# Kernel optimization log

Measured on AMD Instinct MI355X. Metric: run time of the kernel, lower is better.

The kernel has to match this reference:

```python
import jax, jax.numpy as jnp
import numpy as np

# pywt Wavelet('db4') decomposition filters (8 taps)
DEC_LO = jnp.array([-0.010597401784997278, 0.032883011666982945, 0.030841381835986965,
                    -0.18703481171888114, -0.02798376941698385, 0.6308807679295904,
                    0.7148465705525415, 0.23037781330885523], dtype=jnp.float32)
DEC_HI = jnp.array([-0.23037781330885523, 0.7148465705525415, -0.6308807679295904,
                    -0.02798376941698385, 0.18703481171888114, 0.030841381835986965,
                    -0.032883011666982945, -0.010597401784997278], dtype=jnp.float32)
FLEN = 8
LEVEL = 3


def _dwt_last(x, f):
    """Single-level DWT along last axis, pywt 'symmetric' mode.
    out[i] = sum_k f[k] * ext[2i+1-k] (true convolution, downsample by 2)."""
    p = FLEN - 1
    pad = [(0, 0)] * (x.ndim - 1) + [(p, p)]
    xp = jnp.pad(x, pad, mode='symmetric')[..., 1:]
    n = x.shape[-1]
    out_len = (n + FLEN - 1) // 2
    f_rev = f[::-1]
    y = f_rev[0] * xp[..., 0:2 * out_len:2]
    for j in range(1, FLEN):  # fixed 8-tap loop
        y = y + f_rev[j] * xp[..., j:j + 2 * out_len:2]
    return y


def _dwt_h(x, f):
    # DWT along axis -2 (rows/H)
    return jnp.swapaxes(_dwt_last(jnp.swapaxes(x, -1, -2), f), -1, -2)


def _dwt2(x):
    # x: [B, H, W] -> (cA, cH, cV, cD), matching pywt dwt2 ('aa','da','ad','dd')
    lo_w = _dwt_last(x, DEC_LO)
    hi_w = _dwt_last(x, DEC_HI)
    cA = _dwt_h(lo_w, DEC_LO)  # low H,  low W
    cH = _dwt_h(lo_w, DEC_HI)  # high H, low W  (horizontal detail)
    cV = _dwt_h(hi_w, DEC_LO)  # low H,  high W (vertical detail)
    cD = _dwt_h(hi_w, DEC_HI)  # high H, high W (diagonal detail)
    return cA, cH, cV, cD


def setup_inputs() -> dict:
    key = jax.random.key(0)
    x = jax.random.normal(key, (16, 1, 1024, 1024), dtype=jnp.float32)
    return {"x": x}


def reference(x):
    # wavedec2 ordering: (cA_L, (cH_L, cV_L, cD_L), ..., (cH_1, cV_1, cD_1))
    a = x[:, 0]  # [B, H, W]
    details = []
    for _ in range(LEVEL):
        a, lh, hl, hh = _dwt2(a)
        details.insert(0, (lh, hl, hh))  # coarsest first, as pywt returns
    outs = [a[:, None]]  # [B,1,h,w]
    for lh, hl, hh in details:
        outs += [lh[:, None], hl[:, None], hh[:, None]]
    return tuple(outs)
```

## Files before the change

kernel.cpp:

```cpp
#include <hip/hip_runtime.h>

typedef float f4 __attribute__((ext_vector_type(4)));
typedef f4 f4u __attribute__((aligned(4)));

__device__ __forceinline__ int refl(int i, int n) {
    i = (i < 0) ? (-i - 1) : i;
    i = (i >= n) ? (2 * n - 1 - i) : i;
    return i;
}

__device__ __forceinline__ unsigned bpack(float lo, float hi) {
    union { float f; unsigned u; } a, b;
    a.f = lo; b.f = hi;
    const unsigned ua = (a.u + 0x7FFFu + ((a.u >> 16) & 1u)) >> 16;
    const unsigned ub = (b.u + 0x7FFFu + ((b.u >> 16) & 1u)) & 0xFFFF0000u;
    return ua | ub;
}
__device__ __forceinline__ float b_lo(unsigned u) {
    union { unsigned u; float f; } x; x.u = u << 16; return x.f;
}
__device__ __forceinline__ float b_hi(unsigned u) {
    union { unsigned u; float f; } x; x.u = u & 0xFFFF0000u; return x.f;
}

__device__ __constant__ const float LOF[8] = {
    -0.010597401784997278f,  0.032883011666982945f,
     0.030841381835986965f, -0.18703481171888114f,
    -0.02798376941698385f,   0.6308807679295904f,
     0.7148465705525415f,    0.23037781330885523f };
__device__ __constant__ const float HIF[8] = {
    -0.23037781330885523f,   0.7148465705525415f,
    -0.6308807679295904f,   -0.02798376941698385f,
     0.18703481171888114f,   0.030841381835986965f,
    -0.032883011666982945f, -0.010597401784997278f };

template<int N, int LDIN, int M>
__global__ __launch_bounds__(256, 3)
void dwt_stripe(const float* __restrict__ in, int inb,
                float* __restrict__ oA, int ldA, int Ab,
                float* __restrict__ oH, float* __restrict__ oV,
                float* __restrict__ oD)
{
    constexpr int NG  = (M + 7) / 8;
    constexpr int LDP = 8 * NG;
    constexpr int S   = (M + 3) / 4;
    constexpr int NA  = 14 * NG;
    constexpr int NQF = M / 4;
    constexpr int TC  = M - 4 * NQF;
    constexpr int NB  = 2 * NQF + 2 * TC;

    __shared__ unsigned s[14 * LDP];

    const int G = gridDim.x;
    const int q = G >> 3, rm = G & 7;
    const int xcd = blockIdx.x & 7, pos = blockIdx.x >> 3;
    const int sid = xcd * q + (xcd < rm ? xcd : rm) + pos;
    const int sy = sid % S, b = sid / S;

    const int tid = threadIdx.x;
    const int gr0 = 4 * sy;
    const int rb  = 2 * gr0 - 6;
    const float* Ain = in + b * inb;

    #pragma unroll
    for (int k = 0; k < (NA + 255) / 256; ++k) {
        const int item = k * 256 + tid;
        if (item < NA) {
            const int trow = item / NG, g = item - trow * NG;
            const int ri = rb + trow;
            const int cb = 16 * g - 8;
            float v[24];
            if (ri >= 0 && ri < N && g >= 1 && 16 * g + 15 < N) {
                const float* p = Ain + ri * LDIN + cb;
                #pragma unroll
                for (int j = 0; j < 6; ++j) {
                    const float4 t4 = *(const float4*)(p + 4 * j);
                    v[4*j] = t4.x; v[4*j+1] = t4.y; v[4*j+2] = t4.z; v[4*j+3] = t4.w;
                }
            } else {
                const float* row = Ain + refl(ri, N) * LDIN;
                #pragma unroll
                for (int u = 0; u < 24; ++u) v[u] = row[refl(cb + u, N)];
            }
            unsigned w[8];
            #pragma unroll
            for (int d = 0; d < 8; ++d) {
                float lo = 0.f, hi = 0.f;
                #pragma unroll
                for (int t = 0; t < 8; ++t) {
                    const float x = v[2 * d + 9 - t];
                    lo += LOF[t] * x;
                    hi += HIF[t] * x;
                }
                w[d] = bpack(lo, hi);
            }
            unsigned* dst = &s[trow * LDP + 8 * g];
            *(uint4*)(dst)     = make_uint4(w[0], w[1], w[2], w[3]);
            *(uint4*)(dst + 4) = make_uint4(w[4], w[5], w[6], w[7]);
        }
    }
    __syncthreads();

    #pragma unroll
    for (int k = 0; k < (NB + 255) / 256; ++k) {
        const int item = k * 256 + tid;
        if (item < 2 * NQF) {
            const int pr = item / NQF, qc = item - pr * NQF;
            uint4 qv[10];
            #pragma unroll
            for (int j = 0; j < 10; ++j)
                qv[j] = *(const uint4*)&s[(4 * pr + j) * LDP + 4 * qc];

            #pragma unroll
            for (int d = 0; d < 2; ++d) {
                const int gr = gr0 + 2 * pr + d;
                if (gr >= M) continue;
                f4 vA = 0.f, vH = 0.f, vV = 0.f, vD = 0.f;
                #pragma unroll
                for (int t = 0; t < 8; ++t) {
                    const uint4 qq = qv[2 * d + 7 - t];
                    f4 lo, hi;
                    lo.x = b_lo(qq.x); lo.y = b_lo(qq.y); lo.z = b_lo(qq.z); lo.w = b_lo(qq.w);
                    hi.x = b_hi(qq.x); hi.y = b_hi(qq.y); hi.z = b_hi(qq.z); hi.w = b_hi(qq.w);
                    vA += LOF[t] * lo;  vH += HIF[t] * lo;
                    vV += LOF[t] * hi;  vD += HIF[t] * hi;
                }
                const int cq = 4 * qc;
                *(f4u*)&oA[b * Ab + gr * ldA + cq] = vA;
                const int od = b * (M * M) + gr * M + cq;
                *(f4u*)&oH[od] = vH;
                *(f4u*)&oV[od] = vV;
                *(f4u*)&oD[od] = vD;
            }
        } else if (item < NB) {
            const int e = item - 2 * NQF;
            const int pr = e & 1, c = 4 * NQF + (e >> 1);
            float lov[10], hiv[10];
            #pragma unroll
            for (int j = 0; j < 10; ++j) {
                const unsigned u = s[(4 * pr + j) * LDP + c];
                lov[j] = b_lo(u); hiv[j] = b_hi(u);
            }
            float A0=0.f,H0=0.f,V0=0.f,D0=0.f,A1=0.f,H1=0.f,V1=0.f,D1=0.f;
            #pragma unroll
            for (int t = 0; t < 8; ++t) {
                const float l0 = lov[7 - t], h0 = hiv[7 - t];
                const float l1 = lov[9 - t], h1 = hiv[9 - t];
                A0 += LOF[t] * l0;  H0 += HIF[t] * l0;
                V0 += LOF[t] * h0;  D0 += HIF[t] * h0;
                A1 += LOF[t] * l1;  H1 += HIF[t] * l1;
                V1 += LOF[t] * h1;  D1 += HIF[t] * h1;
            }
            const int gr = gr0 + 2 * pr;
            const int od = b * (M * M) + gr * M + c;
            if (gr < M) {
                oA[b * Ab + gr * ldA + c] = A0;
                oH[od] = H0; oV[od] = V0; oD[od] = D0;
            }
            if (gr + 1 < M) {
                oA[b * Ab + (gr + 1) * ldA + c] = A1;
                oH[od + M] = H1; oV[od + M] = V1; oD[od + M] = D1;
            }
        }
    }
}

#define NTF 512
__global__ __launch_bounds__(NTF, 8)
void dwt2_fused(const float* __restrict__ in, int n, int ldin, int inb,
                int m, int nty, int ntx,
                float* __restrict__ oA, int ldA, int Ab,
                float* __restrict__ oH, float* __restrict__ oV,
                float* __restrict__ oD)
{
    __shared__ unsigned s[70 * 36];

    const int G = gridDim.x;
    const int q = G >> 3, rm = G & 7;
    const int xcd = blockIdx.x & 7, pos = blockIdx.x >> 3;
    const int i = xcd * q + (xcd < rm ? xcd : rm) + pos;
    const int ty = i % nty;
    const int t2 = i / nty;
    const int tx = t2 % ntx;
    const int b  = t2 / ntx;

    const int tid = threadIdx.x;
    const int c0 = tx * 32, r0 = ty * 32;
    const float* Ain = in + b * inb;

    const int rb  = 2 * r0 - 6;
    const int cw0 = 2 * c0 - 8;
    const bool interior = (rb >= 0) && (rb + 69 < n) && (cw0 >= 0) && (cw0 + 71 < n);

    const int tr0 = tid >> 3, g0 = tid & 7;
    const bool has2 = (tid < 48);
    const int tr1 = 64 + (tid >> 3), g1 = tid & 7;

    float v0[16], v1[16];
    if (interior) {
        const float* p0 = Ain + (rb + tr0) * ldin + (cw0 + 8 * g0);
        const float4 a0 = ((const float4*)p0)[0];
        const float4 a1 = ((const float4*)p0)[1];
        const float4 a2 = ((const float4*)p0)[2];
        const float4 a3 = ((const float4*)p0)[3];
        v0[0]=a0.x; v0[1]=a0.y; v0[2]=a0.z; v0[3]=a0.w;
        v0[4]=a1.x; v0[5]=a1.y; v0[6]=a1.z; v0[7]=a1.w;
        v0[8]=a2.x; v0[9]=a2.y; v0[10]=a2.z; v0[11]=a2.w;
        v0[12]=a3.x; v0[13]=a3.y; v0[14]=a3.z; v0[15]=a3.w;
        if (has2) {
            const float* p1 = Ain + (rb + tr1) * ldin + (cw0 + 8 * g1);
            const float4 b0 = ((const float4*)p1)[0];
            const float4 b1 = ((const float4*)p1)[1];
            const float4 b2 = ((const float4*)p1)[2];
            const float4 b3 = ((const float4*)p1)[3];
            v1[0]=b0.x; v1[1]=b0.y; v1[2]=b0.z; v1[3]=b0.w;
            v1[4]=b1.x; v1[5]=b1.y; v1[6]=b1.z; v1[7]=b1.w;
            v1[8]=b2.x; v1[9]=b2.y; v1[10]=b2.z; v1[11]=b2.w;
            v1[12]=b3.x; v1[13]=b3.y; v1[14]=b3.z; v1[15]=b3.w;
        }
    } else {
        const float* row0 = Ain + refl(rb + tr0, n) * ldin;
        const int cb0 = cw0 + 8 * g0;
        #pragma unroll
        for (int u = 0; u < 16; ++u) v0[u] = row0[refl(cb0 + u, n)];
        if (has2) {
            const float* row1 = Ain + refl(rb + tr1, n) * ldin;
            const int cb1 = cw0 + 8 * g1;
            #pragma unroll
            for (int u = 0; u < 16; ++u) v1[u] = row1[refl(cb1 + u, n)];
        }
    }

    {
        unsigned w[4];
        #pragma unroll
        for (int d = 0; d < 4; ++d) {
            float lo = 0.f, hi = 0.f;
            #pragma unroll
            for (int t = 0; t < 8; ++t) {
                const float x = v0[2 * d + 9 - t];
                lo += LOF[t] * x;
                hi += HIF[t] * x;
            }
            w[d] = bpack(lo, hi);
        }
        *(uint4*)&s[tr0 * 36 + 4 * g0] = make_uint4(w[0], w[1], w[2], w[3]);
    }
    if (has2) {
        unsigned w[4];
        #pragma unroll
        for (int d = 0; d < 4; ++d) {
            float lo = 0.f, hi = 0.f;
            #pragma unroll
            for (int t = 0; t < 8; ++t) {
                const float x = v1[2 * d + 9 - t];
                lo += LOF[t] * x;
                hi += HIF[t] * x;
            }
            w[d] = bpack(lo, hi);
        }
        *(uint4*)&s[tr1 * 36 + 4 * g1] = make_uint4(w[0], w[1], w[2], w[3]);
    }
    __syncthreads();

    const int c = tid & 31, pr = tid >> 5;
    float lov[10], hiv[10];
    #pragma unroll
    for (int j = 0; j < 10; ++j) {
        const unsigned u = s[(4 * pr + j) * 36 + c];
        lov[j] = b_lo(u); hiv[j] = b_hi(u);
    }
    float A0=0.f,H0=0.f,V0=0.f,D0=0.f,A1=0.f,H1=0.f,V1=0.f,D1=0.f;
    #pragma unroll
    for (int t = 0; t < 8; ++t) {
        const float l0 = lov[7 - t], h0 = hiv[7 - t];
        const float l1 = lov[9 - t], h1 = hiv[9 - t];
        A0 += LOF[t] * l0;  H0 += HIF[t] * l0;
        V0 += LOF[t] * h0;  D0 += HIF[t] * h0;
        A1 += LOF[t] * l1;  H1 += HIF[t] * l1;
        V1 += LOF[t] * h1;  D1 += HIF[t] * h1;
    }
    const int gr = r0 + 2 * pr, gc = c0 + c;
    if (gc < m) {
        const int ob = b * (m * m);
        const int od = ob + gr * m + gc;
        if (gr < m) {
            oA[b * Ab + gr * ldA + gc] = A0;
            oH[od] = H0; oV[od] = V0; oD[od] = D0;
        }
        if (gr + 1 < m) {
            oA[b * Ab + (gr + 1) * ldA + gc] = A1;
            oH[od + m] = H1; oV[od + m] = V1; oD[od + m] = D1;
        }
    }
}

extern "C" void kernel_launch(void* const* d_in, const int* in_sizes, int n_in,
                              void* d_out, int out_size, void* d_ws, size_t ws_size,
                              hipStream_t stream) {
    const float* x = (const float*)d_in[0];
    float* out = (float*)d_out;
    float* ws  = (float*)d_ws;

    const int B = 16;
    const int m1 = 515, m2 = 261, m3 = 134;
    const int n2 = 515, n3 = 261;

    const int ld1 = 516, b1 = m1 * ld1;
    const int ld2 = 264, b2 = m2 * ld2;
    float* a1 = ws;
    float* a2 = ws + (size_t)b1 * B;

    const size_t sz1 = (size_t)B * m1 * m1;
    const size_t sz2 = (size_t)B * m2 * m2;
    const size_t sz3 = (size_t)B * m3 * m3;

    float* a3  = out;
    float* lh3 = a3  + sz3;
    float* hl3 = lh3 + sz3;
    float* hh3 = hl3 + sz3;
    float* lh2 = hh3 + sz3;
    float* hl2 = lh2 + sz2;
    float* hh2 = hl2 + sz2;
    float* lh1 = hh2 + sz2;
    float* hl1 = lh1 + sz1;
    float* hh1 = hl1 + sz1;

    const int S1 = (m1 + 3) / 4;
    const int t2_ = (m2 + 31) / 32;
    const int t3  = (m3 + 31) / 32;

    dim3 blk(256);
    dwt_stripe<1024, 1024, 515><<<dim3(S1 * B), blk, 0, stream>>>(
        x, 1024 * 1024, a1, ld1, b1, lh1, hl1, hh1);

    dwt2_fused<<<dim3(t2_ * t2_ * B), dim3(NTF), 0, stream>>>(
        a1, n2, ld1, b1, m2, t2_, t2_,
        a2, ld2, b2, lh2, hl2, hh2);

    dwt2_fused<<<dim3(t3 * t3 * B), dim3(NTF), 0, stream>>>(
        a2, n3, ld2, b2, m3, t3, t3,
        a3, m3, m3 * m3, lh3, hl3, hh3);
}
```

Baseline: 56.75 us.

## Process eight output rows per stripe block and split interior/edge loads

The first-level stripe kernel is parameterised by rows per block and now computes 8 output rows instead of 4. This cuts the redundant 6-row vertical halo recomputed by each block relative to useful rows. The horizontal pass is also split so interior column groups always take the vectorised float4 path with only row reflection, and the two edge groups use the scalar reflected path. The cost is more shared memory per block (22 rows) and half as many blocks, which may reduce occupancy or parallelism.

```diff
diff --git a/kernel.cpp b/kernel.cpp
--- a/kernel.cpp
+++ b/kernel.cpp
@@ -34,7 +34,7 @@
      0.18703481171888114f,   0.030841381835986965f,
     -0.032883011666982945f, -0.010597401784997278f };
 
-template<int N, int LDIN, int M>
+template<int N, int LDIN, int M, int RPB>
 __global__ __launch_bounds__(256, 3)
 void dwt_stripe(const float* __restrict__ in, int inb,
                 float* __restrict__ oA, int ldA, int Ab,
@@ -43,13 +43,20 @@
 {
     constexpr int NG  = (M + 7) / 8;
     constexpr int LDP = 8 * NG;
-    constexpr int S   = (M + 3) / 4;
-    constexpr int NA  = 14 * NG;
+    constexpr int S   = (M + RPB - 1) / RPB;
+    constexpr int HR  = 2 * RPB + 6;
+    constexpr int GHI = (N - 16) / 16;
+    constexpr int NGI = GHI;
+    static_assert(NG - 1 == GHI + 1, "expect exactly 2 edge groups");
+    constexpr int NAI = HR * NGI;
+    constexpr int NAT = NAI + HR * 2;
     constexpr int NQF = M / 4;
     constexpr int TC  = M - 4 * NQF;
-    constexpr int NB  = 2 * NQF + 2 * TC;
-
-    __shared__ unsigned s[14 * LDP];
+    constexpr int NBM = (RPB / 2) * NQF;
+    constexpr int NBT2 = (RPB / 2) * TC;
+    constexpr int NB  = NBM + NBT2;
+
+    __shared__ unsigned s[HR * LDP];
 
     const int G = gridDim.x;
     const int q = G >> 3, rm = G & 7;
@@ -58,29 +65,23 @@
     const int sy = sid % S, b = sid / S;
 
     const int tid = threadIdx.x;
-    const int gr0 = 4 * sy;
+    const int gr0 = RPB * sy;
     const int rb  = 2 * gr0 - 6;
     const float* Ain = in + b * inb;
 
     #pragma unroll
-    for (int k = 0; k < (NA + 255) / 256; ++k) {
+    for (int k = 0; k < (NAT + 255) / 256; ++k) {
         const int item = k * 256 + tid;
-        if (item < NA) {
-            const int trow = item / NG, g = item - trow * NG;
-            const int ri = rb + trow;
-            const int cb = 16 * g - 8;
+        if (item < NAI) {
+            const int tr = item / NGI;
+            const int g  = 1 + (item - tr * NGI);
+            const int rr = refl(rb + tr, N);
+            const float* p = Ain + rr * LDIN + (16 * g - 8);
             float v[24];
-            if (ri >= 0 && ri < N && g >= 1 && 16 * g + 15 < N) {
-                const float* p = Ain + ri * LDIN + cb;
-                #pragma unroll
-                for (int j = 0; j < 6; ++j) {
-                    const float4 t4 = *(const float4*)(p + 4 * j);
-                    v[4*j] = t4.x; v[4*j+1] = t4.y; v[4*j+2] = t4.z; v[4*j+3] = t4.w;
-                }
-            } else {
-                const float* row = Ain + refl(ri, N) * LDIN;
-                #pragma unroll
-                for (int u = 0; u < 24; ++u) v[u] = row[refl(cb + u, N)];
+            #pragma unroll
+            for (int j = 0; j < 6; ++j) {
+                const float4 t4 = *(const float4*)(p + 4 * j);
+                v[4*j] = t4.x; v[4*j+1] = t4.y; v[4*j+2] = t4.z; v[4*j+3] = t4.w;
             }
             unsigned w[8];
             #pragma unroll
@@ -94,7 +95,32 @@
                 }
                 w[d] = bpack(lo, hi);
             }
-            unsigned* dst = &s[trow * LDP + 8 * g];
+            unsigned* dst = &s[tr * LDP + 8 * g];
+            *(uint4*)(dst)     = make_uint4(w[0], w[1], w[2], w[3]);
+            *(uint4*)(dst + 4) = make_uint4(w[4], w[5], w[6], w[7]);
+        } else if (item < NAT) {
+            const int e  = item - NAI;
+            const int tr = e >> 1;
+            const int g  = (e & 1) ? (GHI + 1) : 0;
+            const int rr = refl(rb + tr, N);
+            const float* row = Ain + rr * LDIN;
+            const int cb = 16 * g - 8;
+            float v[24];
+            #pragma unroll
+            for (int u = 0; u < 24; ++u) v[u] = row[refl(cb + u, N)];
+            unsigned w[8];
+            #pragma unroll
+            for (int d = 0; d < 8; ++d) {
+                float lo = 0.f, hi = 0.f;
+                #pragma unroll
+                for (int t = 0; t < 8; ++t) {
+                    const float x = v[2 * d + 9 - t];
+                    lo += LOF[t] * x;
+                    hi += HIF[t] * x;
+                }
+                w[d] = bpack(lo, hi);
+            }
+            unsigned* dst = &s[tr * LDP + 8 * g];
             *(uint4*)(dst)     = make_uint4(w[0], w[1], w[2], w[3]);
             *(uint4*)(dst + 4) = make_uint4(w[4], w[5], w[6], w[7]);
         }
@@ -104,7 +130,7 @@
     #pragma unroll
     for (int k = 0; k < (NB + 255) / 256; ++k) {
         const int item = k * 256 + tid;
-        if (item < 2 * NQF) {
+        if (item < NBM) {
             const int pr = item / NQF, qc = item - pr * NQF;
             uint4 qv[10];
             #pragma unroll
@@ -133,8 +159,8 @@
                 *(f4u*)&oD[od] = vD;
             }
         } else if (item < NB) {
-            const int e = item - 2 * NQF;
-            const int pr = e & 1, c = 4 * NQF + (e >> 1);
+            const int e = item - NBM;
+            const int pr = e % (RPB / 2), c = 4 * NQF + e / (RPB / 2);
             float lov[10], hiv[10];
             #pragma unroll
             for (int j = 0; j < 10; ++j) {
@@ -326,12 +352,12 @@
     float* hl1 = lh1 + sz1;
     float* hh1 = hl1 + sz1;
 
-    const int S1 = (m1 + 3) / 4;
+    const int S1 = (m1 + 7) / 8;
     const int t2_ = (m2 + 31) / 32;
     const int t3  = (m3 + 31) / 32;
 
     dim3 blk(256);
-    dwt_stripe<1024, 1024, 515><<<dim3(S1 * B), blk, 0, stream>>>(
+    dwt_stripe<1024, 1024, 515, 8><<<dim3(S1 * B), blk, 0, stream>>>(
         x, 1024 * 1024, a1, ld1, b1, lh1, hl1, hh1);
 
     dwt2_fused<<<dim3(t2_ * t2_ * B), dim3(NTF), 0, stream>>>(
```

Measured after the change: 52.39 us, median of 4. 7.7% less time.
